# Optimization experiments

Hardware: AMD Instinct MI355X
Metric: run time of the kernel (lower is better)

The kernel has to match this reference:

```python
import jax, jax.numpy as jnp
import numpy as np
from jax import lax

LEAK = 0.2  # LeakyReLU negative slope used both in flow_conv and as act_type


def conv2d(x, w, b):
    # x: (N,Cin,H,W), w: (Cout,Cin,kh,kw) -> 'SAME' padding, stride 1
    out = lax.conv_general_dilated(x, w, (1, 1), 'SAME',
                                   dimension_numbers=('NCHW', 'OIHW', 'NCHW'))
    return out + b[None, :, None, None]


def leaky(x):
    return jnp.where(x >= 0, x, LEAK * x)


def bilinear_sample(im, ix, iy):
    # im: (C,H,W); ix,iy: (H,W) absolute pixel coords; zero padding (grid_sample default)
    C, H, W = im.shape
    x0 = jnp.floor(ix)
    y0 = jnp.floor(iy)

    def gather(xi, yi):
        valid = (xi >= 0) & (xi <= W - 1) & (yi >= 0) & (yi <= H - 1)
        xc = jnp.clip(xi, 0, W - 1).astype(jnp.int32)
        yc = jnp.clip(yi, 0, H - 1).astype(jnp.int32)
        return im[:, yc, xc] * valid[None].astype(im.dtype)

    wx1 = ix - x0
    wy1 = iy - y0
    wx0 = 1.0 - wx1
    wy0 = 1.0 - wy1
    return (gather(x0, y0) * (wx0 * wy0)[None]
            + gather(x0 + 1, y0) * (wx1 * wy0)[None]
            + gather(x0, y0 + 1) * (wx0 * wy1)[None]
            + gather(x0 + 1, y0 + 1) * (wx1 * wy1)[None])


def warp_all(h, flows):
    # h: (B,Ch,H,W); flows: (B,L,2,H,W). Matches warp(prev_h, -flow) with
    # torch F.grid_sample (bilinear, zero padding, align_corners=False).
    B, Ch, H, W = h.shape
    dt = h.dtype
    xx = jnp.arange(W, dtype=dt)
    yy = jnp.arange(H, dtype=dt)
    vx = xx[None, None, None, :] - flows[:, :, 0]  # grid + (-flow), x coord
    vy = yy[None, None, :, None] - flows[:, :, 1]
    xn = 2.0 * vx / max(W - 1, 1) - 1.0  # normalize to [-1,1]
    yn = 2.0 * vy / max(H - 1, 1) - 1.0
    ix = ((xn + 1.0) * W - 1.0) * 0.5  # unnormalize, align_corners=False
    iy = ((yn + 1.0) * H - 1.0) * 0.5
    samp = jax.vmap(jax.vmap(bilinear_sample, in_axes=(None, 0, 0)),
                    in_axes=(0, 0, 0))
    out = samp(h, ix, iy)  # (B,L,Ch,H,W)
    return out.reshape(B, -1, H, W)  # (B, L*Ch, H, W), same order as torch.cat


def setup_inputs() -> dict:
    key = jax.random.key(0)
    ks = jax.random.split(key, 8)
    B, S, C, H, W = 4, 6, 8, 96, 96
    Ch, L = 64, 13
    sc = lambda fan_in: 1.0 / np.sqrt(fan_in)
    return {
        'inputs': jax.random.normal(ks[0], (B, S, C, H, W), jnp.float32),
        'states': jnp.zeros((B, Ch, H, W), jnp.float32),
        'fw1': jax.random.normal(ks[1], (32, C + Ch, 3, 3), jnp.float32) * sc((C + Ch) * 9),
        'fb1': jnp.zeros((32,), jnp.float32),
        'fw2': jax.random.normal(ks[2], (2 * L, 32, 3, 3), jnp.float32) * sc(32 * 9),
        'fb2': jnp.zeros((2 * L,), jnp.float32),
        'i2h_w': jax.random.normal(ks[3], (3 * Ch, C, 3, 3), jnp.float32) * sc(C * 9),
        'i2h_b': jnp.zeros((3 * Ch,), jnp.float32),
        'ret_w': jax.random.normal(ks[4], (3 * Ch, L * Ch, 1, 1), jnp.float32) * sc(L * Ch),
        'ret_b': jnp.zeros((3 * Ch,), jnp.float32),
        'seq_len': 6,
    }


def reference(inputs, states, fw1, fb1, fw2, fb2, i2h_w, i2h_b, ret_w, ret_b, seq_len):
    B, S, C, H, W = inputs.shape
    Ch = states.shape[1]
    # precompute i2h over all timesteps (as in the torch module)
    i2h = conv2d(inputs.reshape(B * S, C, H, W), i2h_w, i2h_b)
    i2h = i2h.reshape(B, S, 3 * Ch, H, W)

    def step(h, xs):
        x_t, i2h_t = xs  # (B,C,H,W), (B,3Ch,H,W)
        f = leaky(conv2d(jnp.concatenate([x_t, h], axis=1), fw1, fb1))
        flows = conv2d(f, fw2, fb2)  # (B, 2L, H, W)
        flows = flows.reshape(B, flows.shape[1] // 2, 2, H, W)
        warped = warp_all(h, flows)  # (B, L*Ch, H, W)
        h2h = conv2d(warped, ret_w, ret_b)  # (B, 3Ch, H, W)
        i1, i2, i3 = jnp.split(i2h_t, 3, axis=1)
        h1, h2, h3 = jnp.split(h2h, 3, axis=1)
        r = jax.nn.sigmoid(i1 + h1)
        u = jax.nn.sigmoid(i2 + h2)
        m = leaky(i3 + r * h3)
        nh = u * h + (1.0 - u) * m
        return nh, nh

    xs = (jnp.moveaxis(inputs, 0, 1), jnp.moveaxis(i2h, 0, 1))  # time-major
    last_h, outs = lax.scan(step, states, xs)
    return jnp.moveaxis(outs, 0, 1), last_h  # ((B,S,Ch,H,W), (B,Ch,H,W))
```

## Files before the change

kernel.cpp:

```cpp
#include <hip/hip_runtime.h>
#include <hip/hip_bf16.h>
#include <math.h>

#define Bn 4
#define Sn 6
#define Cin 8
#define Hh 96
#define Ww 96
#define HW (Hh*Ww)
#define Chn 64
#define Ln 13
#define LCh (Ln*Chn)
#define OC3 (3*Chn)
#define LEAK 0.2f

typedef __hip_bfloat16 bf16;
typedef __attribute__((ext_vector_type(8))) short short8v;
typedef __attribute__((ext_vector_type(4))) short short4v;
typedef __attribute__((ext_vector_type(4))) float f32x4;

__device__ __forceinline__ float b2f(bf16 v){ return __bfloat162float(v); }
__device__ __forceinline__ bf16  f2b(float v){ return __float2bfloat16(v); }
__device__ __forceinline__ unsigned short bbits(bf16 v){ union{bf16 b; unsigned short s;} u; u.b=v; return u.s; }
__device__ __forceinline__ float us2f(unsigned short u){
    union{unsigned int i; float f;} x; x.i = ((unsigned)u)<<16; return x.f;
}

__device__ __forceinline__ int4 mk_meta(float fx, float fy, int xc, int y){
    float ix = ((float)xc - fx) * (96.0f/95.0f) - 0.5f;
    float iy = ((float)y  - fy) * (96.0f/95.0f) - 0.5f;
    float x0f = floorf(ix), y0f = floorf(iy);
    float wx1 = ix - x0f,  wy1 = iy - y0f;
    float wx0 = 1.f - wx1, wy0 = 1.f - wy1;
    float vx0 = (x0f >=  0.f && x0f <= 95.f) ? 1.f : 0.f;
    float vx1 = (x0f >= -1.f && x0f <= 94.f) ? 1.f : 0.f;
    float vy0 = (y0f >=  0.f && y0f <= 95.f) ? 1.f : 0.f;
    float vy1 = (y0f >= -1.f && y0f <= 94.f) ? 1.f : 0.f;
    int xi0 = (int)fminf(fmaxf(x0f,      0.f), 95.f);
    int xi1 = (int)fminf(fmaxf(x0f+1.f,  0.f), 95.f);
    int yi0 = (int)fminf(fmaxf(y0f,      0.f), 95.f);
    int yi1 = (int)fminf(fmaxf(y0f+1.f,  0.f), 95.f);
    union { _Float16 h[2]; int i; } pz, pw;
    pz.h[0] = (_Float16)(wx0*wy0*vx0*vy0);
    pz.h[1] = (_Float16)(wx1*wy0*vx1*vy0);
    pw.h[0] = (_Float16)(wx0*wy1*vx0*vy1);
    pw.h[1] = (_Float16)(wx1*wy1*vx1*vy1);
    int4 m;
    m.x = (yi0*Ww+xi0) | ((yi0*Ww+xi1)<<16);
    m.y = (yi1*Ww+xi0) | ((yi1*Ww+xi1)<<16);
    m.z = pz.i; m.w = pw.i;
    return m;
}

__global__ void k_prep(const float* __restrict__ fw1, const float* __restrict__ fw2,
                       const float* __restrict__ wi,  const float* __restrict__ rw,
                       bf16* __restrict__ W1b, bf16* __restrict__ W2b,
                       bf16* __restrict__ Wi,  bf16* __restrict__ Wb)
{
    int i = blockIdx.x*256 + threadIdx.x;
    if (i < 21504){
        int oc = i/672, k = i%672; float v = 0.f;
        if (k < 648){ int tap = k/72, ic = k%72; v = fw1[(size_t)oc*648 + ic*9 + tap]; }
        W1b[i] = f2b(v);
    } else if (i < 30720){
        int j = i-21504; int oc = j/288, k = j%288; float v = 0.f;
        if (oc < 26){ int tap = k/32, ic = k%32; v = fw2[(size_t)oc*288 + ic*9 + tap]; }
        W2b[j] = f2b(v);
    } else if (i < 49152){
        int j = i-30720; int oc = j/96, k = j%96; float v = 0.f;
        if (k < 72){ int tap = k/8, ic = k%8; v = wi[(size_t)oc*72 + ic*9 + tap]; }
        Wi[j] = f2b(v);
    } else if (i < 208896){
        int j = i-49152; Wb[j] = f2b(rw[j]);
    }
}

__global__ void k_packx(const float* __restrict__ x, bf16* __restrict__ x_hwc)
{
    __shared__ unsigned short tx[8][68];
    int bs = blockIdx.y, pix0 = blockIdx.x*64, tid = threadIdx.x;
    #pragma unroll
    for (int it=0; it<2; ++it){
        int idx = it*256 + tid, ic = idx>>6, p = idx&63;
        tx[ic][p] = bbits(f2b(x[((size_t)bs*Cin + ic)*HW + pix0 + p]));
    }
    __syncthreads();
    unsigned short* dst = (unsigned short*)x_hwc;
    #pragma unroll
    for (int it=0; it<2; ++it){
        int j = it*256 + tid, p = j>>3, c = j&7;
        dst[((size_t)bs*HW + pix0 + p)*8 + c] = tx[c][p];
    }
}

__global__ void k_packh0(const float* __restrict__ s, bf16* __restrict__ hwc)
{
    __shared__ unsigned short t[64][65];
    int b = blockIdx.y, pix0 = blockIdx.x*64, tid = threadIdx.x;
    unsigned short* dst = (unsigned short*)hwc;
    #pragma unroll
    for (int it=0; it<16; ++it){
        int idx = it*256 + tid, c = idx>>6, p = idx&63;
        t[c][p] = bbits(f2b(s[((size_t)b*Chn + c)*HW + pix0 + p]));
    }
    __syncthreads();
    #pragma unroll
    for (int it=0; it<16; ++it){
        int idx = it*256 + tid, p = idx>>6, c = idx&63;
        dst[((size_t)b*HW + pix0 + p)*Chn + c] = t[c][p];
    }
}

__global__ __launch_bounds__(384) void k_front(const bf16* __restrict__ x_hwc,
        const bf16* __restrict__ h_hwc,
        const bf16* __restrict__ Wi,  const float* __restrict__ ib,
        const bf16* __restrict__ W1b, const float* __restrict__ fb1,
        bf16* __restrict__ i2h_hwc, bf16* __restrict__ f_hwc, int t)
{
    __shared__ bf16 tile[3*98*72];
    int y = blockIdx.x, b = blockIdx.y, tid = threadIdx.x;
    const bf16* xb = x_hwc + (size_t)(b*Sn + t)*HW*8;
    const bf16* hb = h_hwc + (size_t)b*HW*64;
    for (int s = tid; s < 294; s += 384){
        int r = s/98, px = s%98 - 1, yy = y + r - 1;
        float4* dst = (float4*)&tile[s*72];
        if (yy>=0 && yy<Hh && px>=0 && px<Ww){
            size_t gp = (size_t)yy*Ww + px;
            dst[0] = *(const float4*)(xb + gp*8);
            const float4* hsrc = (const float4*)(hb + gp*64);
            #pragma unroll
            for (int q=0;q<8;++q) dst[1+q] = hsrc[q];
        } else {
            float4 z{0,0,0,0};
            #pragma unroll
            for (int q=0;q<9;++q) dst[q] = z;
        }
    }
    __syncthreads();
    int wv = tid>>6, lane = tid&63, x0 = wv*16, n = lane&15, kg = lane>>4;
    int pix = y*Ww + x0 + n;

    {
        f32x4 acc[12];
        #pragma unroll
        for (int m=0;m<12;++m) acc[m] = f32x4{0,0,0,0};
        #pragma unroll
        for (int kk=0; kk<3; ++kk){
            int g = kk*4 + kg;
            int tap = (g > 8) ? 8 : g;
            int dy = tap/3, dx = tap%3;
            short8v bv = *(const short8v*)&tile[((dy*98) + (x0+n) + dx)*72];
            #pragma unroll
            for (int m=0;m<12;++m){
                short8v av = *(const short8v*)(Wi + (size_t)(m*16 + n)*96 + g*8);
                acc[m] = __builtin_amdgcn_mfma_f32_16x16x32_bf16(av, bv, acc[m], 0,0,0);
            }
        }
        size_t prow = ((size_t)b*HW + pix)*192;
        #pragma unroll
        for (int m=0;m<12;++m){
            short4v sv;
            #pragma unroll
            for (int r=0;r<4;++r){
                int oc = m*16 + kg*4 + r;
                sv[r] = (short)bbits(f2b(acc[m][r] + ib[oc]));
            }
            *(short4v*)&i2h_hwc[prow + m*16 + kg*4] = sv;
        }
    }

    {
        f32x4 acc0{0,0,0,0}, acc1{0,0,0,0};
        #pragma unroll
        for (int kk=0; kk<21; ++kk){
            int g = kk*4 + kg;
            int gc = (g > 80) ? 80 : g;
            int tap = gc/9, ch0 = (gc%9)*8;
            int dy = tap/3, dx = tap%3;
            short8v bv = *(const short8v*)&tile[(((dy*98) + (x0+n) + dx))*72 + ch0];
            short8v a0 = *(const short8v*)(W1b + (size_t)n*672 + g*8);
            short8v a1 = *(const short8v*)(W1b + (size_t)(16+n)*672 + g*8);
            acc0 = __builtin_amdgcn_mfma_f32_16x16x32_bf16(a0, bv, acc0, 0,0,0);
            acc1 = __builtin_amdgcn_mfma_f32_16x16x32_bf16(a1, bv, acc1, 0,0,0);
        }
        size_t prow = (size_t)b*HW + pix;
        #pragma unroll
        for (int mt=0; mt<2; ++mt){
            f32x4 a = mt ? acc1 : acc0;
            short4v sv;
            #pragma unroll
            for (int r=0;r<4;++r){
                int oc = mt*16 + kg*4 + r;
                float v = a[r] + fb1[oc];
                sv[r] = (short)bbits(f2b((v >= 0.f) ? v : LEAK*v));
            }
            *(short4v*)&f_hwc[prow*32 + mt*16 + kg*4] = sv;
        }
    }
}

__global__ __launch_bounds__(384) void k_conv2meta(const bf16* __restrict__ f_hwc,
        const bf16* __restrict__ W2b, const float* __restrict__ fb2,
        int4* __restrict__ meta)
{
    __shared__ bf16 tile[3*98*32];
    int y = blockIdx.x, b = blockIdx.y, tid = threadIdx.x;
    const bf16* fb = f_hwc + (size_t)b*HW*32;
    for (int s = tid; s < 294; s += 384){
        int r = s/98, px = s%98 - 1, yy = y + r - 1;
        float4* dst = (float4*)&tile[s*32];
        if (yy>=0 && yy<Hh && px>=0 && px<Ww){
            const float4* src = (const float4*)(fb + ((size_t)yy*Ww + px)*32);
            #pragma unroll
            for (int q=0;q<4;++q) dst[q] = src[q];
        } else {
            float4 z{0,0,0,0};
            #pragma unroll
            for (int q=0;q<4;++q) dst[q] = z;
        }
    }
    __syncthreads();
    int wv = tid>>6, lane = tid&63, x0 = wv*16, n = lane&15, kg = lane>>4;
    f32x4 acc0{0,0,0,0}, acc1{0,0,0,0};
    #pragma unroll
    for (int kk=0; kk<9; ++kk){
        int g = kk*4 + kg;
        int tap = g>>2, ch0 = (g&3)*8;
        int dy = tap/3, dx = tap%3;
        short8v bv = *(const short8v*)&tile[(((dy*98) + (x0+n) + dx))*32 + ch0];
        short8v a0 = *(const short8v*)(W2b + (size_t)n*288 + g*8);
        short8v a1 = *(const short8v*)(W2b + (size_t)(16+n)*288 + g*8);
        acc0 = __builtin_amdgcn_mfma_f32_16x16x32_bf16(a0, bv, acc0, 0,0,0);
        acc1 = __builtin_amdgcn_mfma_f32_16x16x32_bf16(a1, bv, acc1, 0,0,0);
    }
    int xc = x0 + n, pix = y*Ww + xc;
    int4* mb = meta + (size_t)b*Ln*HW + pix;
    {
        float v0 = acc0[0] + fb2[kg*4+0], v1 = acc0[1] + fb2[kg*4+1];
        float v2 = acc0[2] + fb2[kg*4+2], v3 = acc0[3] + fb2[kg*4+3];
        mb[(size_t)(2*kg  )*HW] = mk_meta(v0, v1, xc, y);
        mb[(size_t)(2*kg+1)*HW] = mk_meta(v2, v3, xc, y);
    }
    if (kg < 3){
        float v0 = acc1[0] + fb2[16+kg*4+0], v1 = acc1[1] + fb2[16+kg*4+1];
        mb[(size_t)(8+2*kg)*HW] = mk_meta(v0, v1, xc, y);
        if (kg < 2){
            float v2 = acc1[2] + fb2[16+kg*4+2], v3 = acc1[3] + fb2[16+kg*4+3];
            mb[(size_t)(9+2*kg)*HW] = mk_meta(v2, v3, xc, y);
        }
    }
}

__global__ __launch_bounds__(256) void k_fused(const int4* __restrict__ meta,
        const bf16* __restrict__ h_cur, const bf16* __restrict__ Wb,
        const float* __restrict__ rb, const bf16* __restrict__ i2h_hwc,
        bf16* __restrict__ h_nxt, float* __restrict__ out, int t)
{
    __shared__ bf16 wlds[32*LCh];
    char* ldsb = (char*)wlds;
    int tid = threadIdx.x, wv = tid>>6, lane = tid&63;
    int b = blockIdx.y, pix0 = blockIdx.x*32;
    const bf16* hb = h_cur + (size_t)b*HW*64;
    const unsigned short* hsu = (const unsigned short*)hb;
    const int4* mb = meta + (size_t)b*Ln*HW + pix0;

    int px = lane & 31;
    int oh = lane >> 5;
    int pswz = (px&7)<<4;
    for (int l = wv; l < Ln; l += 4){
        int4 m = mb[(size_t)l*HW + px];
        int o00 = m.x & 0xFFFF, o10 = ((unsigned)m.x) >> 16;
        int o01 = m.y & 0xFFFF, o11 = ((unsigned)m.y) >> 16;
        union { int i; _Float16 h[2]; } uz, uw;
        uz.i = m.z; uw.i = m.w;
        float w00 = (float)uz.h[0], w10 = (float)uz.h[1];
        float w01 = (float)uw.h[0], w11 = (float)uw.h[1];
        #pragma unroll
        for (int o2 = 0; o2 < 4; ++o2){
            int oct = o2*2 + oh;
            const unsigned short* s00 = hsu + (size_t)o00*64 + oct*8;
            const unsigned short* s10 = hsu + (size_t)o10*64 + oct*8;
            const unsigned short* s01 = hsu + (size_t)o01*64 + oct*8;
            const unsigned short* s11 = hsu + (size_t)o11*64 + oct*8;
            short8v v00 = *(const short8v*)s00;
            short8v v10 = *(const short8v*)s10;
            short8v v01 = *(const short8v*)s01;
            short8v v11 = *(const short8v*)s11;
            short8v r8;
            #pragma unroll
            for (int k=0;k<8;++k){
                float v = us2f((unsigned short)v00[k])*w00
                        + us2f((unsigned short)v10[k])*w10
                        + us2f((unsigned short)v01[k])*w01
                        + us2f((unsigned short)v11[k])*w11;
                r8[k] = (short)bbits(f2b(v));
            }
            *(short8v*)(ldsb + px*1664 + ((l*128 + oct*16) ^ pswz)) = r8;
        }
    }

    int col = lane & 15, kg = lane >> 4;
    int pxa = pix0 + col, pxb = pxa + 16;
    short4v hva = *(const short4v*)&hb[(size_t)pxa*64 + wv*16 + kg*4];
    short4v hvb = *(const short4v*)&hb[(size_t)pxb*64 + wv*16 + kg*4];
    const bf16* ia = i2h_hwc + ((size_t)b*HW + pxa)*192 + wv*16 + kg*4;
    const bf16* ibp= i2h_hwc + ((size_t)b*HW + pxb)*192 + wv*16 + kg*4;
    short4v i1a = *(const short4v*)(ia);
    short4v i2a = *(const short4v*)(ia + 64);
    short4v i3a = *(const short4v*)(ia + 128);
    short4v i1b = *(const short4v*)(ibp);
    short4v i2b = *(const short4v*)(ibp + 64);
    short4v i3b = *(const short4v*)(ibp + 128);
    __syncthreads();

    const short8v* a0 = (const short8v*)(Wb + (size_t)((wv+0)*16+col)*LCh + kg*8);
    const short8v* a1 = (const short8v*)(Wb + (size_t)((wv+4)*16+col)*LCh + kg*8);
    const short8v* a2 = (const short8v*)(Wb + (size_t)((wv+8)*16+col)*LCh + kg*8);
    f32x4 c0a{0,0,0,0}, c1a{0,0,0,0}, c2a{0,0,0,0};
    f32x4 c0b{0,0,0,0}, c1b{0,0,0,0}, c2b{0,0,0,0};
    int swz = (col&7)<<4;
    #pragma unroll 2
    for (int kk=0; kk<26; ++kk){
        short8v av0 = a0[kk*4], av1 = a1[kk*4], av2 = a2[kk*4];
        int offa = col*1664 + ((kk*64 + kg*16) ^ swz);
        int offb = (col+16)*1664 + ((kk*64 + kg*16) ^ ((col&7)<<4));
        short8v bva = *(const short8v*)(ldsb + offa);
        short8v bvb = *(const short8v*)(ldsb + offb);
        c0a = __builtin_amdgcn_mfma_f32_16x16x32_bf16(av0, bva, c0a, 0,0,0);
        c0b = __builtin_amdgcn_mfma_f32_16x16x32_bf16(av0, bvb, c0b, 0,0,0);
        c1a = __builtin_amdgcn_mfma_f32_16x16x32_bf16(av1, bva, c1a, 0,0,0);
        c1b = __builtin_amdgcn_mfma_f32_16x16x32_bf16(av1, bvb, c1b, 0,0,0);
        c2a = __builtin_amdgcn_mfma_f32_16x16x32_bf16(av2, bva, c2a, 0,0,0);
        c2b = __builtin_amdgcn_mfma_f32_16x16x32_bf16(av2, bvb, c2b, 0,0,0);
    }

    float nha[4], nhb[4];
    #pragma unroll
    for (int r=0; r<4; ++r){
        int cc = wv*16 + kg*4 + r;
        float h1 = c0a[r] + rb[cc];
        float h2 = c1a[r] + rb[cc+64];
        float h3 = c2a[r] + rb[cc+128];
        float rg = 1.f/(1.f + expf(-(us2f((unsigned short)i1a[r]) + h1)));
        float u  = 1.f/(1.f + expf(-(us2f((unsigned short)i2a[r]) + h2)));
        float mp = us2f((unsigned short)i3a[r]) + rg*h3;
        float m  = (mp >= 0.f) ? mp : LEAK*mp;
        float nh = u*us2f((unsigned short)hva[r]) + (1.f - u)*m;
        nha[r] = nh;
        out[(((size_t)(b*Sn+t))*Chn + cc)*HW + pxa] = nh;
        if (t == Sn-1)
            out[(size_t)Bn*Sn*Chn*HW + ((size_t)b*Chn + cc)*HW + pxa] = nh;
    }
    #pragma unroll
    for (int r=0; r<4; ++r){
        int cc = wv*16 + kg*4 + r;
        float h1 = c0b[r] + rb[cc];
        float h2 = c1b[r] + rb[cc+64];
        float h3 = c2b[r] + rb[cc+128];
        float rg = 1.f/(1.f + expf(-(us2f((unsigned short)i1b[r]) + h1)));
        float u  = 1.f/(1.f + expf(-(us2f((unsigned short)i2b[r]) + h2)));
        float mp = us2f((unsigned short)i3b[r]) + rg*h3;
        float m  = (mp >= 0.f) ? mp : LEAK*mp;
        float nh = u*us2f((unsigned short)hvb[r]) + (1.f - u)*m;
        nhb[r] = nh;
        out[(((size_t)(b*Sn+t))*Chn + cc)*HW + pxb] = nh;
        if (t == Sn-1)
            out[(size_t)Bn*Sn*Chn*HW + ((size_t)b*Chn + cc)*HW + pxb] = nh;
    }
    short4v sva, svb;
    #pragma unroll
    for (int r=0; r<4; ++r){
        sva[r] = (short)bbits(f2b(nha[r]));
        svb[r] = (short)bbits(f2b(nhb[r]));
    }
    *(short4v*)&h_nxt[((size_t)b*HW + pxa)*64 + wv*16 + kg*4] = sva;
    *(short4v*)&h_nxt[((size_t)b*HW + pxb)*64 + wv*16 + kg*4] = svb;
}

extern "C" void kernel_launch(void* const* d_in, const int* in_sizes, int n_in,
                              void* d_out, int out_size, void* d_ws, size_t ws_size,
                              hipStream_t stream) {
    const float* inputs = (const float*)d_in[0];
    const float* states = (const float*)d_in[1];
    const float* fw1    = (const float*)d_in[2];
    const float* fb1    = (const float*)d_in[3];
    const float* fw2    = (const float*)d_in[4];
    const float* fb2    = (const float*)d_in[5];
    const float* i2h_w  = (const float*)d_in[6];
    const float* i2h_b  = (const float*)d_in[7];
    const float* ret_w  = (const float*)d_in[8];
    const float* ret_b  = (const float*)d_in[9];
    float* out = (float*)d_out;

    char* ws = (char*)d_ws;
    bf16* h_hwcA  = (bf16*)(ws);
    bf16* h_hwcB  = (bf16*)(ws +  4718592);
    bf16* x_hwc   = (bf16*)(ws +  9437184);
    bf16* i2h_hwc = (bf16*)(ws + 12976128);
    bf16* f_hwc   = (bf16*)(ws + 27131904);
    int4* meta    = (int4*)(ws + 29491200);
    bf16* W1b     = (bf16*)(ws + 37158912);
    bf16* W2b     = (bf16*)(ws + 37201920);
    bf16* Wi      = (bf16*)(ws + 37220352);
    bf16* Wb      = (bf16*)(ws + 37257216);

    k_prep  <<<dim3(816),        256, 0, stream>>>(fw1, fw2, i2h_w, ret_w,
                                                   W1b, W2b, Wi, Wb);
    k_packx <<<dim3(144, Bn*Sn), 256, 0, stream>>>(inputs, x_hwc);
    k_packh0<<<dim3(144, Bn),    256, 0, stream>>>(states, h_hwcA);

    bf16* h_cur = h_hwcA;
    bf16* h_nxt = h_hwcB;
    for (int t = 0; t < Sn; ++t) {
        k_front    <<<dim3(96, Bn),  384, 0, stream>>>(x_hwc, h_cur, Wi, i2h_b,
                                                       W1b, fb1, i2h_hwc, f_hwc, t);
        k_conv2meta<<<dim3(96, Bn),  384, 0, stream>>>(f_hwc, W2b, fb2, meta);
        k_fused    <<<dim3(288, Bn), 256, 0, stream>>>(meta, h_cur, Wb, ret_b,
                                                       i2h_hwc, h_nxt, out, t);
        bf16* tmp = h_cur; h_cur = h_nxt; h_nxt = tmp;
    }
}
```

Baseline: 722.3 us.

## Build warped MFMA operands in registers instead of staging them through LDS

The fused warp plus h2h-GEMM kernel no longer writes the bilinearly warped hidden state into a 53KB shared-memory tile. Each wave now gathers and interpolates its own pixel-major A fragments per k-step and feeds them straight into MFMA, with the weights as the B operand. The block shrinks to 128 threads with no barrier, and output stores become float4 along pixels. The cost is that each of the two waves redoes the full bilinear gather for the block's 32 pixels, and the h_nxt and i2h accesses become scalar, strided loads and stores.

```diff
diff --git a/kernel.cpp b/kernel.cpp
--- a/kernel.cpp
+++ b/kernel.cpp
@@ -251,41 +251,50 @@
     }
 }
 
-__global__ __launch_bounds__(256) void k_fused(const int4* __restrict__ meta,
+__global__ __launch_bounds__(128) void k_fused(const int4* __restrict__ meta,
         const bf16* __restrict__ h_cur, const bf16* __restrict__ Wb,
         const float* __restrict__ rb, const bf16* __restrict__ i2h_hwc,
         bf16* __restrict__ h_nxt, float* __restrict__ out, int t)
 {
-    __shared__ bf16 wlds[32*LCh];
-    char* ldsb = (char*)wlds;
     int tid = threadIdx.x, wv = tid>>6, lane = tid&63;
     int b = blockIdx.y, pix0 = blockIdx.x*32;
+    int col = lane & 15, kg = lane >> 4;
+    int nb = wv*2;
     const bf16* hb = h_cur + (size_t)b*HW*64;
     const unsigned short* hsu = (const unsigned short*)hb;
     const int4* mb = meta + (size_t)b*Ln*HW + pix0;
 
-    int px = lane & 31;
-    int oh = lane >> 5;
-    int pswz = (px&7)<<4;
-    for (int l = wv; l < Ln; l += 4){
-        int4 m = mb[(size_t)l*HW + px];
-        int o00 = m.x & 0xFFFF, o10 = ((unsigned)m.x) >> 16;
-        int o01 = m.y & 0xFFFF, o11 = ((unsigned)m.y) >> 16;
-        union { int i; _Float16 h[2]; } uz, uw;
-        uz.i = m.z; uw.i = m.w;
-        float w00 = (float)uz.h[0], w10 = (float)uz.h[1];
-        float w01 = (float)uw.h[0], w11 = (float)uw.h[1];
-        #pragma unroll
-        for (int o2 = 0; o2 < 4; ++o2){
-            int oct = o2*2 + oh;
-            const unsigned short* s00 = hsu + (size_t)o00*64 + oct*8;
-            const unsigned short* s10 = hsu + (size_t)o10*64 + oct*8;
-            const unsigned short* s01 = hsu + (size_t)o01*64 + oct*8;
-            const unsigned short* s11 = hsu + (size_t)o11*64 + oct*8;
-            short8v v00 = *(const short8v*)s00;
-            short8v v10 = *(const short8v*)s10;
-            short8v v01 = *(const short8v*)s01;
-            short8v v11 = *(const short8v*)s11;
+    const bf16* brow0 = Wb + (size_t)((nb+0)*16 + col)*LCh + kg*8;
+    const bf16* brow1 = Wb + (size_t)((nb+1)*16 + col)*LCh + kg*8;
+    const bf16* brow2 = Wb + (size_t)((nb+4)*16 + col)*LCh + kg*8;
+    const bf16* brow3 = Wb + (size_t)((nb+5)*16 + col)*LCh + kg*8;
+    const bf16* brow4 = Wb + (size_t)((nb+8)*16 + col)*LCh + kg*8;
+    const bf16* brow5 = Wb + (size_t)((nb+9)*16 + col)*LCh + kg*8;
+
+    f32x4 acc[2][6];
+    #pragma unroll
+    for (int m=0;m<2;++m)
+        #pragma unroll
+        for (int j=0;j<6;++j) acc[m][j] = f32x4{0,0,0,0};
+
+    #pragma unroll
+    for (int kk=0; kk<26; ++kk){
+        int l = kk>>1;
+        int c0 = (kk&1)*32 + kg*8;
+        short8v af0, af1;
+        #pragma unroll
+        for (int m=0;m<2;++m){
+            int4 mm = mb[(size_t)l*HW + m*16 + col];
+            int o00 = mm.x & 0xFFFF, o10 = ((unsigned)mm.x) >> 16;
+            int o01 = mm.y & 0xFFFF, o11 = ((unsigned)mm.y) >> 16;
+            union { int i; _Float16 h[2]; } uz, uw;
+            uz.i = mm.z; uw.i = mm.w;
+            float w00 = (float)uz.h[0], w10 = (float)uz.h[1];
+            float w01 = (float)uw.h[0], w11 = (float)uw.h[1];
+            short8v v00 = *(const short8v*)(hsu + (size_t)o00*64 + c0);
+            short8v v10 = *(const short8v*)(hsu + (size_t)o10*64 + c0);
+            short8v v01 = *(const short8v*)(hsu + (size_t)o01*64 + c0);
+            short8v v11 = *(const short8v*)(hsu + (size_t)o11*64 + c0);
             short8v r8;
             #pragma unroll
             for (int k=0;k<8;++k){
@@ -295,86 +304,62 @@
                         + us2f((unsigned short)v11[k])*w11;
                 r8[k] = (short)bbits(f2b(v));
             }
-            *(short8v*)(ldsb + px*1664 + ((l*128 + oct*16) ^ pswz)) = r8;
-        }
-    }
-
-    int col = lane & 15, kg = lane >> 4;
-    int pxa = pix0 + col, pxb = pxa + 16;
-    short4v hva = *(const short4v*)&hb[(size_t)pxa*64 + wv*16 + kg*4];
-    short4v hvb = *(const short4v*)&hb[(size_t)pxb*64 + wv*16 + kg*4];
-    const bf16* ia = i2h_hwc + ((size_t)b*HW + pxa)*192 + wv*16 + kg*4;
-    const bf16* ibp= i2h_hwc + ((size_t)b*HW + pxb)*192 + wv*16 + kg*4;
-    short4v i1a = *(const short4v*)(ia);
-    short4v i2a = *(const short4v*)(ia + 64);
-    short4v i3a = *(const short4v*)(ia + 128);
-    short4v i1b = *(const short4v*)(ibp);
-    short4v i2b = *(const short4v*)(ibp + 64);
-    short4v i3b = *(const short4v*)(ibp + 128);
-    __syncthreads();
-
-    const short8v* a0 = (const short8v*)(Wb + (size_t)((wv+0)*16+col)*LCh + kg*8);
-    const short8v* a1 = (const short8v*)(Wb + (size_t)((wv+4)*16+col)*LCh + kg*8);
-    const short8v* a2 = (const short8v*)(Wb + (size_t)((wv+8)*16+col)*LCh + kg*8);
-    f32x4 c0a{0,0,0,0}, c1a{0,0,0,0}, c2a{0,0,0,0};
-    f32x4 c0b{0,0,0,0}, c1b{0,0,0,0}, c2b{0,0,0,0};
-    int swz = (col&7)<<4;
-    #pragma unroll 2
-    for (int kk=0; kk<26; ++kk){
-        short8v av0 = a0[kk*4], av1 = a1[kk*4], av2 = a2[kk*4];
-        int offa = col*1664 + ((kk*64 + kg*16) ^ swz);
-        int offb = (col+16)*1664 + ((kk*64 + kg*16) ^ ((col&7)<<4));
-        short8v bva = *(const short8v*)(ldsb + offa);
-        short8v bvb = *(const short8v*)(ldsb + offb);
-        c0a = __builtin_amdgcn_mfma_f32_16x16x32_bf16(av0, bva, c0a, 0,0,0);
-        c0b = __builtin_amdgcn_mfma_f32_16x16x32_bf16(av0, bvb, c0b, 0,0,0);
-        c1a = __builtin_amdgcn_mfma_f32_16x16x32_bf16(av1, bva, c1a, 0,0,0);
-        c1b = __builtin_amdgcn_mfma_f32_16x16x32_bf16(av1, bvb, c1b, 0,0,0);
-        c2a = __builtin_amdgcn_mfma_f32_16x16x32_bf16(av2, bva, c2a, 0,0,0);
-        c2b = __builtin_amdgcn_mfma_f32_16x16x32_bf16(av2, bvb, c2b, 0,0,0);
-    }
-
-    float nha[4], nhb[4];
-    #pragma unroll
-    for (int r=0; r<4; ++r){
-        int cc = wv*16 + kg*4 + r;
-        float h1 = c0a[r] + rb[cc];
-        float h2 = c1a[r] + rb[cc+64];
-        float h3 = c2a[r] + rb[cc+128];
-        float rg = 1.f/(1.f + expf(-(us2f((unsigned short)i1a[r]) + h1)));
-        float u  = 1.f/(1.f + expf(-(us2f((unsigned short)i2a[r]) + h2)));
-        float mp = us2f((unsigned short)i3a[r]) + rg*h3;
-        float m  = (mp >= 0.f) ? mp : LEAK*mp;
-        float nh = u*us2f((unsigned short)hva[r]) + (1.f - u)*m;
-        nha[r] = nh;
-        out[(((size_t)(b*Sn+t))*Chn + cc)*HW + pxa] = nh;
-        if (t == Sn-1)
-            out[(size_t)Bn*Sn*Chn*HW + ((size_t)b*Chn + cc)*HW + pxa] = nh;
-    }
-    #pragma unroll
-    for (int r=0; r<4; ++r){
-        int cc = wv*16 + kg*4 + r;
-        float h1 = c0b[r] + rb[cc];
-        float h2 = c1b[r] + rb[cc+64];
-        float h3 = c2b[r] + rb[cc+128];
-        float rg = 1.f/(1.f + expf(-(us2f((unsigned short)i1b[r]) + h1)));
-        float u  = 1.f/(1.f + expf(-(us2f((unsigned short)i2b[r]) + h2)));
-        float mp = us2f((unsigned short)i3b[r]) + rg*h3;
-        float m  = (mp >= 0.f) ? mp : LEAK*mp;
-        float nh = u*us2f((unsigned short)hvb[r]) + (1.f - u)*m;
-        nhb[r] = nh;
-        out[(((size_t)(b*Sn+t))*Chn + cc)*HW + pxb] = nh;
-        if (t == Sn-1)
-            out[(size_t)Bn*Sn*Chn*HW + ((size_t)b*Chn + cc)*HW + pxb] = nh;
-    }
-    short4v sva, svb;
-    #pragma unroll
-    for (int r=0; r<4; ++r){
-        sva[r] = (short)bbits(f2b(nha[r]));
-        svb[r] = (short)bbits(f2b(nhb[r]));
-    }
-    *(short4v*)&h_nxt[((size_t)b*HW + pxa)*64 + wv*16 + kg*4] = sva;
-    *(short4v*)&h_nxt[((size_t)b*HW + pxb)*64 + wv*16 + kg*4] = svb;
+            if (m == 0) af0 = r8; else af1 = r8;
+        }
+        short8v bf0 = *(const short8v*)(brow0 + kk*32);
+        short8v bf1 = *(const short8v*)(brow1 + kk*32);
+        short8v bf2 = *(const short8v*)(brow2 + kk*32);
+        short8v bf3 = *(const short8v*)(brow3 + kk*32);
+        short8v bf4 = *(const short8v*)(brow4 + kk*32);
+        short8v bf5 = *(const short8v*)(brow5 + kk*32);
+        acc[0][0] = __builtin_amdgcn_mfma_f32_16x16x32_bf16(af0, bf0, acc[0][0], 0,0,0);
+        acc[0][1] = __builtin_amdgcn_mfma_f32_16x16x32_bf16(af0, bf1, acc[0][1], 0,0,0);
+        acc[0][2] = __builtin_amdgcn_mfma_f32_16x16x32_bf16(af0, bf2, acc[0][2], 0,0,0);
+        acc[0][3] = __builtin_amdgcn_mfma_f32_16x16x32_bf16(af0, bf3, acc[0][3], 0,0,0);
+        acc[0][4] = __builtin_amdgcn_mfma_f32_16x16x32_bf16(af0, bf4, acc[0][4], 0,0,0);
+        acc[0][5] = __builtin_amdgcn_mfma_f32_16x16x32_bf16(af0, bf5, acc[0][5], 0,0,0);
+        acc[1][0] = __builtin_amdgcn_mfma_f32_16x16x32_bf16(af1, bf0, acc[1][0], 0,0,0);
+        acc[1][1] = __builtin_amdgcn_mfma_f32_16x16x32_bf16(af1, bf1, acc[1][1], 0,0,0);
+        acc[1][2] = __builtin_amdgcn_mfma_f32_16x16x32_bf16(af1, bf2, acc[1][2], 0,0,0);
+        acc[1][3] = __builtin_amdgcn_mfma_f32_16x16x32_bf16(af1, bf3, acc[1][3], 0,0,0);
+        acc[1][4] = __builtin_amdgcn_mfma_f32_16x16x32_bf16(af1, bf4, acc[1][4], 0,0,0);
+        acc[1][5] = __builtin_amdgcn_mfma_f32_16x16x32_bf16(af1, bf5, acc[1][5], 0,0,0);
+    }
+
+    #pragma unroll
+    for (int m=0;m<2;++m){
+        int pxbase = pix0 + m*16 + kg*4;
+        #pragma unroll
+        for (int jn=0;jn<2;++jn){
+            int cc = (nb+jn)*16 + col;
+            float rbias1 = rb[cc], rbias2 = rb[cc+64], rbias3 = rb[cc+128];
+            float4 ov;
+            #pragma unroll
+            for (int r=0;r<4;++r){
+                int px = pxbase + r;
+                float h1 = acc[m][jn  ][r] + rbias1;
+                float h2 = acc[m][jn+2][r] + rbias2;
+                float h3 = acc[m][jn+4][r] + rbias3;
+                const unsigned short* ip = (const unsigned short*)
+                    (i2h_hwc + ((size_t)b*HW + px)*192 + cc);
+                float i1 = us2f(ip[0]);
+                float i2 = us2f(ip[64]);
+                float i3 = us2f(ip[128]);
+                float hv = us2f(((const unsigned short*)hb)[(size_t)px*64 + cc]);
+                float rg = 1.f/(1.f + expf(-(i1 + h1)));
+                float u  = 1.f/(1.f + expf(-(i2 + h2)));
+                float mp = i3 + rg*h3;
+                float mm2 = (mp >= 0.f) ? mp : LEAK*mp;
+                float nh = u*hv + (1.f - u)*mm2;
+                ((float*)&ov)[r] = nh;
+                h_nxt[((size_t)b*HW + px)*64 + cc] = f2b(nh);
+            }
+            *(float4*)&out[(((size_t)(b*Sn+t))*Chn + cc)*HW + pxbase] = ov;
+            if (t == Sn-1)
+                *(float4*)&out[(size_t)Bn*Sn*Chn*HW
+                               + ((size_t)b*Chn + cc)*HW + pxbase] = ov;
+        }
+    }
 }
 
 extern "C" void kernel_launch(void* const* d_in, const int* in_sizes, int n_in,
@@ -415,7 +400,7 @@
         k_front    <<<dim3(96, Bn),  384, 0, stream>>>(x_hwc, h_cur, Wi, i2h_b,
                                                        W1b, fb1, i2h_hwc, f_hwc, t);
         k_conv2meta<<<dim3(96, Bn),  384, 0, stream>>>(f_hwc, W2b, fb2, meta);
-        k_fused    <<<dim3(288, Bn), 256, 0, stream>>>(meta, h_cur, Wb, ret_b,
+        k_fused    <<<dim3(288, Bn), 128, 0, stream>>>(meta, h_cur, Wb, ret_b,
                                                        i2h_hwc, h_nxt, out, t);
         bf16* tmp = h_cur; h_cur = h_nxt; h_nxt = tmp;
     }
```

After: 954.3 us. 32.1% more time.
